# Kernel tuning notes

Measured on AMD Instinct MI355X. Metric: run time of the kernel, lower is better.

The kernel has to match this reference:

```python
import jax, jax.numpy as jnp
import numpy as np

SELECT_SIZE = 64
SM_SCALE = 0.07216878364870322  # 192 ** -0.5
V_HEAD_DIM = 128


def setup_inputs() -> dict:
    key = jax.random.key(0)
    k1, k2, k3, k4 = jax.random.split(key, 4)
    B, S, Hq, G, TOPK = 4, 2048, 16, 4, 16
    T = B * S
    NB = S // SELECT_SIZE  # 32 blocks per sequence
    q = jax.random.normal(k1, (T, Hq, 192), dtype=jnp.float32)
    k = jax.random.normal(k2, (T, Hq, 192), dtype=jnp.float32)
    v = jax.random.normal(k3, (T, Hq, V_HEAD_DIM), dtype=jnp.float32)
    idx = jax.random.randint(k4, (T, G, TOPK), 0, NB, dtype=jnp.int32)
    # guarantee block 0 is always selected so every causal row has >=1 valid key
    idx = idx.at[..., 0].set(0)
    idx = jnp.sort(idx, axis=-1)
    return {"q": q, "k": k, "v": v, "selected_indices": idx,
            "batch_size": B, "seq_len": S}


def reference(q, k, v, selected_indices, batch_size, seq_len):
    B, S = batch_size, seq_len
    Hq = q.shape[1]
    G = selected_indices.shape[1]
    Hg = Hq // G  # query heads per selection-score group
    nb = (S + SELECT_SIZE - 1) // SELECT_SIZE
    dv = v.shape[-1]

    # un-ragged: B equal-length sequences
    qg = q.reshape(B, S, G, Hg, -1)
    kg = k.reshape(B, S, G, Hg, -1)
    vg = v.reshape(B, S, G, Hg, -1)
    idx = selected_indices.reshape(B, S, G, -1)

    # which KV blocks are selected for each (query position, group): [B,S,G,nb]
    allowed_blk = (idx[..., None] == jnp.arange(nb, dtype=idx.dtype)).any(axis=-2)
    blk_of_pos = jnp.arange(S) // SELECT_SIZE
    pos_ok = allowed_blk[..., blk_of_pos]  # [B, Tq, G, Skv]
    causal = jnp.arange(S)[:, None] >= jnp.arange(S)[None, :]
    mask = pos_ok & causal[None, :, None, :]          # [B, Tq, G, Skv]
    mask = mask.transpose(0, 2, 1, 3)[:, :, None]      # [B, G, 1, Tq, Skv]

    scores = jnp.einsum('btghd,bsghd->bghts', qg, kg) * SM_SCALE
    scores = jnp.where(mask, scores, jnp.float32(-1e30))
    attn = jax.nn.softmax(scores, axis=-1)
    o = jnp.einsum('bghts,bsghd->btghd', attn, vg)
    return o.reshape(B * S, Hq * dv)
```

## Files before the change

### kernel.cpp

```cpp
#include <hip/hip_runtime.h>


typedef __attribute__((ext_vector_type(8))) _Float16 half8;
typedef __attribute__((ext_vector_type(4))) float f32x4;

__device__ __forceinline__ half8 cvt8(const float4* p) {
  float4 a = p[0], b = p[1];
  half8 r;
  r[0] = (_Float16)a.x; r[1] = (_Float16)a.y; r[2] = (_Float16)a.z; r[3] = (_Float16)a.w;
  r[4] = (_Float16)b.x; r[5] = (_Float16)b.y; r[6] = (_Float16)b.z; r[7] = (_Float16)b.w;
  return r;
}

__device__ __forceinline__ half8 cvt8s(const float4* p, float s) {
  float4 a = p[0], b = p[1];
  half8 r;
  r[0] = (_Float16)(a.x * s); r[1] = (_Float16)(a.y * s);
  r[2] = (_Float16)(a.z * s); r[3] = (_Float16)(a.w * s);
  r[4] = (_Float16)(b.x * s); r[5] = (_Float16)(b.y * s);
  r[6] = (_Float16)(b.z * s); r[7] = (_Float16)(b.w * s);
  return r;
}

__device__ __forceinline__ void async16(const void* g, void* l) {
  __builtin_amdgcn_global_load_lds(
      (const __attribute__((address_space(1))) void*)g,
      (__attribute__((address_space(3))) void*)l, 16, 0, 0);
}

template <int CTRL>
__device__ __forceinline__ float dpp_mov(float x) {
  union { float f; int i; } u;
  u.f = x;
  u.i = __builtin_amdgcn_update_dpp(u.i, u.i, CTRL, 0xf, 0xf, true);
  return u.f;
}
__device__ __forceinline__ float row16_max(float r) {
  r = fmaxf(r, dpp_mov<0xB1>(r));
  r = fmaxf(r, dpp_mov<0x4E>(r));
  r = fmaxf(r, dpp_mov<0x141>(r));
  r = fmaxf(r, dpp_mov<0x140>(r));
  return r;
}
__device__ __forceinline__ float row16_sum(float r) {
  r += dpp_mov<0xB1>(r);
  r += dpp_mov<0x4E>(r);
  r += dpp_mov<0x141>(r);
  r += dpp_mov<0x140>(r);
  return r;
}

__global__ __launch_bounds__(256) void kf_prep(const float* __restrict__ k,
                                               _Float16* __restrict__ kf) {
  int O = blockIdx.x * 256 + threadIdx.x;
  int blk = O / 1536;
  int rem = O - blk * 1536;
  int frag = rem >> 6;
  int lane = rem & 63;
  int ntile = frag / 6;
  int kc = frag - ntile * 6;
  int n = ntile * 16 + (lane & 15);
  int d = kc * 32 + (lane >> 4) * 8;
  int bh = blk >> 5, kb = blk & 31;
  int b = bh >> 4, h = bh & 15;
  long t = (long)b * 2048 + kb * 64 + n;
  const float* src = k + (t * 16 + h) * 192 + d;
  *(half8*)(kf + (long)O * 8) = cvt8((const float4*)src);
}

__global__ __launch_bounds__(256) void vf_prep(const float* __restrict__ v,
                                               _Float16* __restrict__ vf) {
  __shared__ float ld[64][132];
  int blk = blockIdx.x;
  int bh = blk >> 5, kb = blk & 31;
  int b = bh >> 4, h = bh & 15;
  int tid = threadIdx.x;
  const float* src = v + ((long)(b * 2048 + kb * 64) * 16 + h) * 128;
#pragma unroll
  for (int it = 0; it < 32; ++it) {
    int id = it * 256 + tid;
    int kk = id >> 7, dv = id & 127;
    ld[kk][dv] = src[(long)kk * 2048 + dv];
  }
  __syncthreads();
  _Float16* dst = vf + (long)blk * 8192;
#pragma unroll
  for (int it = 0; it < 4; ++it) {
    int oct = it * 256 + tid;
    int frag = oct >> 6, lane = oct & 63;
    int n0 = frag >> 1, kc = frag & 1;
    int dv = n0 * 16 + (lane & 15);
    int kbase = kc * 32 + (lane >> 4) * 8;
    half8 o;
#pragma unroll
    for (int j = 0; j < 8; ++j) o[j] = (_Float16)ld[kbase + j][dv];
    *(half8*)(dst + (long)oct * 8) = o;
  }
}

__global__ __launch_bounds__(256) void attn_main(const float* __restrict__ q,
                                                 const int* __restrict__ idx,
                                                 const _Float16* __restrict__ kf,
                                                 const _Float16* __restrict__ vf,
                                                 float* __restrict__ out) {
  constexpr float SCL = 0.07216878364870322f * 1.4426950408889634f;
  int id = (int)blockIdx.x;
  int qb = 31 - (id >> 6);
  int h = id & 15, b = (id >> 4) & 3, g = h >> 2;
  int tid = threadIdx.x;
  int w = tid >> 6, L = tid & 63;
  int Lm = L & 15, Lq = L >> 4;
  int m0 = w * 16;
  int t0 = b * 2048 + qb * 64;

  __shared__ __align__(16) char sh_kv[40960];
  __shared__ __align__(16) _Float16 Pbuf[4][16 * 72];
  __shared__ unsigned un_sh[4];
  char* lk = sh_kv;
  char* lv = sh_kv + 24576;

  half8 qa[6];
  const float* qrow = q + ((long)(t0 + m0 + Lm) * 16 + h) * 192;
#pragma unroll
  for (int c = 0; c < 6; ++c) qa[c] = cvt8s((const float4*)(qrow + c * 32 + Lq * 8), SCL);

  unsigned mrow = 0;
  {
    const int* ip = idx + ((long)(t0 + m0 + Lm) * 4 + g) * 16;
#pragma unroll
    for (int j = 0; j < 16; ++j) mrow |= (1u << ip[j]);
  }
  unsigned un = mrow;
#pragma unroll
  for (int o = 32; o; o >>= 1) un |= __shfl_xor(un, o, 64);
  unsigned smask[4];
#pragma unroll
  for (int i = 0; i < 4; ++i) smask[i] = __shfl(mrow, Lq * 4 + i, 64);
  if (L == 0) un_sh[w] = un;
  __syncthreads();
  unsigned bm = un_sh[0] | un_sh[1] | un_sh[2] | un_sh[3];

  f32x4 Oacc[8];
#pragma unroll
  for (int n0 = 0; n0 < 8; ++n0) Oacc[n0] = (f32x4){0.f, 0.f, 0.f, 0.f};
  float m_i[4] = {-1e30f, -1e30f, -1e30f, -1e30f};
  float l_i[4] = {0.f, 0.f, 0.f, 0.f};

  const char* kfb = (const char*)(kf + (long)((b * 16 + h) * 32) * 12288);
  const char* vfb = (const char*)(vf + (long)((b * 16 + h) * 32) * 8192);
  _Float16* pw = &Pbuf[w][0];
  const half8* lkf = (const half8*)lk;
  const half8* lvf = (const half8*)lv;

  for (int kb = 0; kb <= qb; ++kb) {
    if (!((bm >> kb) & 1u)) continue;

    {
      const char* kg = kfb + (long)kb * 24576;
      const char* vg = vfb + (long)kb * 16384;
#pragma unroll
      for (int c = 0; c < 6; ++c) {
        int ch = w + c * 4;
        async16(kg + ch * 1024 + L * 16, lk + ch * 1024);
      }
#pragma unroll
      for (int c = 0; c < 4; ++c) {
        int ch = w + c * 4;
        async16(vg + ch * 1024 + L * 16, lv + ch * 1024);
      }
    }
    asm volatile("s_waitcnt vmcnt(0)" ::: "memory");
    __syncthreads();

    if ((un >> kb) & 1u) {
      f32x4 S[4];
#pragma unroll
      for (int nt = 0; nt < 4; ++nt) {
        f32x4 acc = {0.f, 0.f, 0.f, 0.f};
#pragma unroll
        for (int c = 0; c < 6; ++c)
          acc = __builtin_amdgcn_mfma_f32_16x16x32_f16(qa[c], lkf[(nt * 6 + c) * 64 + L], acc, 0, 0, 0);
        S[nt] = acc;
      }

      bool lastb = (kb == qb);
      float rmax[4] = {-1e30f, -1e30f, -1e30f, -1e30f};
      float sc[4][4];
#pragma unroll
      for (int nt = 0; nt < 4; ++nt) {
        int key = nt * 16 + Lm;
#pragma unroll
        for (int i = 0; i < 4; ++i) {
          bool ok = ((smask[i] >> kb) & 1u) && (!lastb || key <= m0 + Lq * 4 + i);
          float val = ok ? S[nt][i] : -1e30f;
          sc[nt][i] = val;
          rmax[i] = fmaxf(rmax[i], val);
        }
      }
      float alpha[4], psum[4];
      _Float16 pf[4][4];
#pragma unroll
      for (int i = 0; i < 4; ++i) {
        float r = row16_max(rmax[i]);
        float mn = fmaxf(m_i[i], r);
        alpha[i] = exp2f(m_i[i] - mn);
        m_i[i] = mn;
        float s = 0.f;
#pragma unroll
        for (int nt = 0; nt < 4; ++nt) {
          float p = exp2f(sc[nt][i] - mn);
          pf[nt][i] = (_Float16)p;
          s += p;
        }
        psum[i] = s;
      }
#pragma unroll
      for (int i = 0; i < 4; ++i) l_i[i] = l_i[i] * alpha[i] + row16_sum(psum[i]);
#pragma unroll
      for (int n0 = 0; n0 < 8; ++n0)
#pragma unroll
        for (int i = 0; i < 4; ++i) Oacc[n0][i] *= alpha[i];

      asm volatile("s_waitcnt lgkmcnt(0)" ::: "memory");
#pragma unroll
      for (int nt = 0; nt < 4; ++nt)
#pragma unroll
        for (int i = 0; i < 4; ++i)
          pw[(Lq * 4 + i) * 72 + nt * 16 + Lm] = pf[nt][i];
      asm volatile("s_waitcnt lgkmcnt(0)" ::: "memory");

#pragma unroll
      for (int kc = 0; kc < 2; ++kc) {
        half8 afr = *(const half8*)(pw + Lm * 72 + kc * 32 + Lq * 8);
#pragma unroll
        for (int n0 = 0; n0 < 8; ++n0)
          Oacc[n0] = __builtin_amdgcn_mfma_f32_16x16x32_f16(afr, lvf[(n0 * 2 + kc) * 64 + L], Oacc[n0], 0, 0, 0);
      }
    }
    __syncthreads();
  }

#pragma unroll
  for (int i = 0; i < 4; ++i) l_i[i] = 1.f / l_i[i];
  float* orow = out + (long)(t0 + m0 + Lq * 4) * 2048 + h * 128 + Lm;
#pragma unroll
  for (int i = 0; i < 4; ++i)
#pragma unroll
    for (int n0 = 0; n0 < 8; ++n0)
      orow[(long)i * 2048 + n0 * 16] = Oacc[n0][i] * l_i[i];
}

extern "C" void kernel_launch(void* const* d_in, const int* in_sizes, int n_in,
                              void* d_out, int out_size, void* d_ws, size_t ws_size,
                              hipStream_t stream) {
  const float* q = (const float*)d_in[0];
  const float* k = (const float*)d_in[1];
  const float* v = (const float*)d_in[2];
  const int* idx = (const int*)d_in[3];
  _Float16* kf = (_Float16*)d_ws;
  _Float16* vf = kf + (size_t)4 * 16 * 32 * 12288;
  float* out = (float*)d_out;
  kf_prep<<<12288, 256, 0, stream>>>(k, kf);
  vf_prep<<<2048, 256, 0, stream>>>(v, vf);
  attn_main<<<2048, 256, 0, stream>>>(q, idx, kf, vf, out);
}
```

Measured before the change: 452.6 us.

## Fuse K/V prep kernels and specialize non-diagonal softmax path with lazy rescale

Merges the K and V fp16 fragment-packing kernels into one launch that stages K through shared memory with coalesced float4 loads, then reuses the same buffer for V. In the attention loop, non-diagonal blocks take a simplified softmax: no causal compare, selection applied as a multiplier, and the running-max rescale of O and l skipped unless some row's max grows. The diagonal block is peeled out of the loop, and hardware exp2 builtins replace exp2f. This cuts launch overhead, uncoalesced K reads and per-block VALU work, at the cost of extra control flow and a wave-wide vote per block.

```diff
diff --git a/kernel.cpp b/kernel.cpp
--- a/kernel.cpp
+++ b/kernel.cpp
@@ -50,51 +50,56 @@
   return r;
 }
 
-__global__ __launch_bounds__(256) void kf_prep(const float* __restrict__ k,
-                                               _Float16* __restrict__ kf) {
-  int O = blockIdx.x * 256 + threadIdx.x;
-  int blk = O / 1536;
-  int rem = O - blk * 1536;
-  int frag = rem >> 6;
-  int lane = rem & 63;
-  int ntile = frag / 6;
-  int kc = frag - ntile * 6;
-  int n = ntile * 16 + (lane & 15);
-  int d = kc * 32 + (lane >> 4) * 8;
-  int bh = blk >> 5, kb = blk & 31;
-  int b = bh >> 4, h = bh & 15;
-  long t = (long)b * 2048 + kb * 64 + n;
-  const float* src = k + (t * 16 + h) * 192 + d;
-  *(half8*)(kf + (long)O * 8) = cvt8((const float4*)src);
-}
-
-__global__ __launch_bounds__(256) void vf_prep(const float* __restrict__ v,
+__global__ __launch_bounds__(256) void kv_prep(const float* __restrict__ k,
+                                               const float* __restrict__ v,
+                                               _Float16* __restrict__ kf,
                                                _Float16* __restrict__ vf) {
-  __shared__ float ld[64][132];
+  __shared__ float lb[64 * 196];
   int blk = blockIdx.x;
   int bh = blk >> 5, kb = blk & 31;
   int b = bh >> 4, h = bh & 15;
   int tid = threadIdx.x;
-  const float* src = v + ((long)(b * 2048 + kb * 64) * 16 + h) * 128;
-#pragma unroll
-  for (int it = 0; it < 32; ++it) {
-    int id = it * 256 + tid;
-    int kk = id >> 7, dv = id & 127;
-    ld[kk][dv] = src[(long)kk * 2048 + dv];
+
+  const float* ksrc = k + ((long)(b * 2048 + kb * 64) * 16 + h) * 192;
+#pragma unroll
+  for (int it = 0; it < 12; ++it) {
+    int idx = it * 256 + tid;
+    int kk = idx / 48, c4 = idx - kk * 48;
+    *(float4*)(&lb[kk * 196 + c4 * 4]) = *(const float4*)(ksrc + (long)kk * 3072 + c4 * 4);
   }
   __syncthreads();
-  _Float16* dst = vf + (long)blk * 8192;
+  _Float16* kdst = kf + (long)blk * 12288;
+#pragma unroll
+  for (int it = 0; it < 6; ++it) {
+    int oct = it * 256 + tid;
+    int frag = oct >> 6, lane = oct & 63;
+    int ntile = frag / 6, kc = frag - ntile * 6;
+    int n = ntile * 16 + (lane & 15);
+    int d = kc * 32 + ((lane >> 4) << 3);
+    *(half8*)(kdst + (long)oct * 8) = cvt8((const float4*)(&lb[n * 196 + d]));
+  }
+  __syncthreads();
+
+  const float* vsrc = v + ((long)(b * 2048 + kb * 64) * 16 + h) * 128;
+#pragma unroll
+  for (int it = 0; it < 8; ++it) {
+    int idx = it * 256 + tid;
+    int kk = idx >> 5, c4 = idx & 31;
+    *(float4*)(&lb[kk * 132 + c4 * 4]) = *(const float4*)(vsrc + (long)kk * 2048 + c4 * 4);
+  }
+  __syncthreads();
+  _Float16* vdst = vf + (long)blk * 8192;
 #pragma unroll
   for (int it = 0; it < 4; ++it) {
     int oct = it * 256 + tid;
     int frag = oct >> 6, lane = oct & 63;
     int n0 = frag >> 1, kc = frag & 1;
     int dv = n0 * 16 + (lane & 15);
-    int kbase = kc * 32 + (lane >> 4) * 8;
+    int kbase = kc * 32 + ((lane >> 4) << 3);
     half8 o;
 #pragma unroll
-    for (int j = 0; j < 8; ++j) o[j] = (_Float16)ld[kbase + j][dv];
-    *(half8*)(dst + (long)oct * 8) = o;
+    for (int j = 0; j < 8; ++j) o[j] = (_Float16)lb[(kbase + j) * 132 + dv];
+    *(half8*)(vdst + (long)oct * 8) = o;
   }
 }
 
@@ -152,38 +157,70 @@
   const half8* lkf = (const half8*)lk;
   const half8* lvf = (const half8*)lv;
 
-  for (int kb = 0; kb <= qb; ++kb) {
-    if (!((bm >> kb) & 1u)) continue;
-
-    {
-      const char* kg = kfb + (long)kb * 24576;
-      const char* vg = vfb + (long)kb * 16384;
-#pragma unroll
-      for (int c = 0; c < 6; ++c) {
-        int ch = w + c * 4;
-        async16(kg + ch * 1024 + L * 16, lk + ch * 1024);
+  auto stage = [&](int kb) {
+    const char* kg = kfb + (long)kb * 24576;
+    const char* vg = vfb + (long)kb * 16384;
+#pragma unroll
+    for (int c = 0; c < 6; ++c) {
+      int ch = w + c * 4;
+      async16(kg + ch * 1024 + L * 16, lk + ch * 1024);
+    }
+#pragma unroll
+    for (int c = 0; c < 4; ++c) {
+      int ch = w + c * 4;
+      async16(vg + ch * 1024 + L * 16, lv + ch * 1024);
+    }
+  };
+
+  auto compute = [&](int kb, bool lastb) __attribute__((always_inline)) {
+    f32x4 S[4];
+#pragma unroll
+    for (int nt = 0; nt < 4; ++nt) {
+      f32x4 acc = {0.f, 0.f, 0.f, 0.f};
+#pragma unroll
+      for (int c = 0; c < 6; ++c)
+        acc = __builtin_amdgcn_mfma_f32_16x16x32_f16(qa[c], lkf[(nt * 6 + c) * 64 + L], acc, 0, 0, 0);
+      S[nt] = acc;
+    }
+
+    _Float16 pf[4][4];
+    if (!lastb) {
+      float msel[4];
+#pragma unroll
+      for (int i = 0; i < 4; ++i) msel[i] = ((smask[i] >> kb) & 1u) ? 1.0f : 0.0f;
+      float rmax[4] = {-1e30f, -1e30f, -1e30f, -1e30f};
+#pragma unroll
+      for (int nt = 0; nt < 4; ++nt)
+#pragma unroll
+        for (int i = 0; i < 4; ++i) rmax[i] = fmaxf(rmax[i], S[nt][i]);
+#pragma unroll
+      for (int i = 0; i < 4; ++i) rmax[i] = row16_max(rmax[i]);
+      bool up = (rmax[0] > m_i[0]) | (rmax[1] > m_i[1]) |
+                (rmax[2] > m_i[2]) | (rmax[3] > m_i[3]);
+      if (__any(up)) {
+        f32x4 av;
+#pragma unroll
+        for (int i = 0; i < 4; ++i) {
+          float mn = fmaxf(m_i[i], rmax[i]);
+          av[i] = __builtin_amdgcn_exp2f(m_i[i] - mn);
+          m_i[i] = mn;
+          l_i[i] *= av[i];
+        }
+#pragma unroll
+        for (int n0 = 0; n0 < 8; ++n0) Oacc[n0] *= av;
       }
-#pragma unroll
-      for (int c = 0; c < 4; ++c) {
-        int ch = w + c * 4;
-        async16(vg + ch * 1024 + L * 16, lv + ch * 1024);
-      }
-    }
-    asm volatile("s_waitcnt vmcnt(0)" ::: "memory");
-    __syncthreads();
-
-    if ((un >> kb) & 1u) {
-      f32x4 S[4];
-#pragma unroll
-      for (int nt = 0; nt < 4; ++nt) {
-        f32x4 acc = {0.f, 0.f, 0.f, 0.f};
-#pragma unroll
-        for (int c = 0; c < 6; ++c)
-          acc = __builtin_amdgcn_mfma_f32_16x16x32_f16(qa[c], lkf[(nt * 6 + c) * 64 + L], acc, 0, 0, 0);
-        S[nt] = acc;
-      }
-
-      bool lastb = (kb == qb);
+      float psum[4] = {0.f, 0.f, 0.f, 0.f};
+#pragma unroll
+      for (int nt = 0; nt < 4; ++nt)
+#pragma unroll
+        for (int i = 0; i < 4; ++i) {
+          float p = __builtin_amdgcn_exp2f(S[nt][i] - m_i[i]) * msel[i];
+          pf[nt][i] = (_Float16)p;
+          psum[i] += p;
+        }
+#pragma unroll
+      for (int i = 0; i < 4; ++i) l_i[i] += row16_sum(psum[i]);
+    } else {
       float rmax[4] = {-1e30f, -1e30f, -1e30f, -1e30f};
       float sc[4][4];
 #pragma unroll
@@ -191,53 +228,65 @@
         int key = nt * 16 + Lm;
 #pragma unroll
         for (int i = 0; i < 4; ++i) {
-          bool ok = ((smask[i] >> kb) & 1u) && (!lastb || key <= m0 + Lq * 4 + i);
+          bool ok = ((smask[i] >> kb) & 1u) && (key <= m0 + Lq * 4 + i);
           float val = ok ? S[nt][i] : -1e30f;
           sc[nt][i] = val;
           rmax[i] = fmaxf(rmax[i], val);
         }
       }
-      float alpha[4], psum[4];
-      _Float16 pf[4][4];
+      f32x4 av;
+      float psum[4];
 #pragma unroll
       for (int i = 0; i < 4; ++i) {
         float r = row16_max(rmax[i]);
         float mn = fmaxf(m_i[i], r);
-        alpha[i] = exp2f(m_i[i] - mn);
+        av[i] = __builtin_amdgcn_exp2f(m_i[i] - mn);
         m_i[i] = mn;
         float s = 0.f;
 #pragma unroll
         for (int nt = 0; nt < 4; ++nt) {
-          float p = exp2f(sc[nt][i] - mn);
+          float p = __builtin_amdgcn_exp2f(sc[nt][i] - mn);
           pf[nt][i] = (_Float16)p;
           s += p;
         }
         psum[i] = s;
       }
 #pragma unroll
-      for (int i = 0; i < 4; ++i) l_i[i] = l_i[i] * alpha[i] + row16_sum(psum[i]);
+      for (int i = 0; i < 4; ++i) l_i[i] = l_i[i] * av[i] + row16_sum(psum[i]);
+#pragma unroll
+      for (int n0 = 0; n0 < 8; ++n0) Oacc[n0] *= av;
+    }
+
+    asm volatile("s_waitcnt lgkmcnt(0)" ::: "memory");
+#pragma unroll
+    for (int nt = 0; nt < 4; ++nt)
+#pragma unroll
+      for (int i = 0; i < 4; ++i)
+        pw[(Lq * 4 + i) * 72 + nt * 16 + Lm] = pf[nt][i];
+    asm volatile("s_waitcnt lgkmcnt(0)" ::: "memory");
+
+#pragma unroll
+    for (int kc = 0; kc < 2; ++kc) {
+      half8 afr = *(const half8*)(pw + Lm * 72 + kc * 32 + Lq * 8);
 #pragma unroll
       for (int n0 = 0; n0 < 8; ++n0)
-#pragma unroll
-        for (int i = 0; i < 4; ++i) Oacc[n0][i] *= alpha[i];
-
-      asm volatile("s_waitcnt lgkmcnt(0)" ::: "memory");
-#pragma unroll
-      for (int nt = 0; nt < 4; ++nt)
-#pragma unroll
-        for (int i = 0; i < 4; ++i)
-          pw[(Lq * 4 + i) * 72 + nt * 16 + Lm] = pf[nt][i];
-      asm volatile("s_waitcnt lgkmcnt(0)" ::: "memory");
-
-#pragma unroll
-      for (int kc = 0; kc < 2; ++kc) {
-        half8 afr = *(const half8*)(pw + Lm * 72 + kc * 32 + Lq * 8);
-#pragma unroll
-        for (int n0 = 0; n0 < 8; ++n0)
-          Oacc[n0] = __builtin_amdgcn_mfma_f32_16x16x32_f16(afr, lvf[(n0 * 2 + kc) * 64 + L], Oacc[n0], 0, 0, 0);
-      }
-    }
+        Oacc[n0] = __builtin_amdgcn_mfma_f32_16x16x32_f16(afr, lvf[(n0 * 2 + kc) * 64 + L], Oacc[n0], 0, 0, 0);
+    }
+  };
+
+  for (int kb = 0; kb < qb; ++kb) {
+    if (!((bm >> kb) & 1u)) continue;
+    stage(kb);
+    asm volatile("s_waitcnt vmcnt(0)" ::: "memory");
     __syncthreads();
+    if ((un >> kb) & 1u) compute(kb, false);
+    __syncthreads();
+  }
+  if ((bm >> qb) & 1u) {
+    stage(qb);
+    asm volatile("s_waitcnt vmcnt(0)" ::: "memory");
+    __syncthreads();
+    if ((un >> qb) & 1u) compute(qb, true);
   }
 
 #pragma unroll
@@ -258,9 +307,8 @@
   const float* v = (const float*)d_in[2];
   const int* idx = (const int*)d_in[3];
   _Float16* kf = (_Float16*)d_ws;
-  _Float16* vf = kf + (size_t)4 * 16 * 32 * 12288;
+  _Float16* vf = kf + (size_t)2048 * 12288;
   float* out = (float*)d_out;
-  kf_prep<<<12288, 256, 0, stream>>>(k, kf);
-  vf_prep<<<2048, 256, 0, stream>>>(v, vf);
+  kv_prep<<<2048, 256, 0, stream>>>(k, v, kf, vf);
   attn_main<<<2048, 256, 0, stream>>>(q, idx, kf, vf, out);
 }
```

Result: faster. 409.0 us (-9.6%).
